# Performance work log

Measured on AMD Instinct MI355X. Metric: run time of the kernel, lower is better.

The kernel has to match this reference:

```python
import jax, jax.numpy as jnp
import numpy as np

SIZE = 128
WIN = SIZE // 4   # sliding-window size == region size (32)
HALF = WIN // 2   # 16


def _conv(x, w, pad, groups=1):
    return jax.lax.conv_general_dilated(x, w, (1, 1), [(pad, pad), (pad, pad)],
        dimension_numbers=('NCHW', 'OIHW', 'NCHW'), feature_group_count=groups)


def _resize(x, h, w):
    # F.interpolate(..., mode='bilinear', align_corners=False)
    return jax.image.resize(x, (x.shape[0], x.shape[1], h, w), 'bilinear', antialias=False)


def _gauss_kernels():
    ax = np.linspace(-2.0, 2.0, 5)
    xx, yy = np.meshgrid(ax, ax)
    g = np.exp(-(xx ** 2 + yy ** 2) / 2.0) / (2.0 * np.pi)  # sigma = 1
    gx = (-xx * g).astype(np.float32)
    gy = (-yy * g).astype(np.float32)
    return (jnp.asarray(np.tile(gx[None, None], (3, 3, 1, 1))),
            jnp.asarray(np.tile(gy[None, None], (3, 3, 1, 1))))


def _edge_extract(x):
    Gx, Gy = _gauss_kernels()
    h = _conv(x, Gx, 2)
    v = _conv(x, Gy, 2)
    return jnp.tanh(jnp.sqrt(h * h + v * v + 1e-8))


def _color_moments(x, win=5):
    # F.unfold-based local mean / unbiased var / skewness, via depthwise box sums
    C = x.shape[1]
    n = float(win * win)
    ones = jnp.ones((C, 1, win, win), x.dtype)
    box = lambda z: _conv(z, ones, win // 2, groups=C)
    s1 = box(x); s2 = box(x * x); s3 = box(x * x * x)
    mean = s1 / n
    var = (s2 - n * mean * mean) / (n - 1.0)               # unbiased, matches torch.var
    m3 = (s3 - 3.0 * mean * s2 + 2.0 * n * mean ** 3) / n  # E[(x-m)^3]
    skew = m3 / (jnp.sqrt(jnp.maximum(var, 0.0)) ** 3 + 1e-6)
    return jnp.concatenate([mean, var, skew], 1)


def _locate_region(c):
    # scipy: gradient magnitude < 0.2 -> 4-connected label at argmax -> bbox center
    H, W = c.shape
    flat = jnp.argmax(c)
    xm = (flat // W).astype(jnp.int32)
    ym = (flat % W).astype(jnp.int32)
    gm = jnp.hypot(jnp.gradient(c, axis=0), jnp.gradient(c, axis=1))
    mask = gm < 0.2
    seed = jnp.zeros((H, W), bool).at[xm, ym].set(True) & mask

    def dil(r):
        d = r
        d = d | jnp.pad(r[1:, :], ((0, 1), (0, 0)))
        d = d | jnp.pad(r[:-1, :], ((1, 0), (0, 0)))
        d = d | jnp.pad(r[:, 1:], ((0, 0), (0, 1)))
        d = d | jnp.pad(r[:, :-1], ((0, 0), (1, 0)))
        return d & mask

    def body(s):
        r, _ = s
        nr = dil(r)
        return (nr, jnp.any(nr != r))

    region, _ = jax.lax.while_loop(lambda s: s[1], body, (seed, jnp.any(seed)))
    rows = jnp.any(region, 1); cols = jnp.any(region, 0)
    rs = jnp.argmax(rows); re = H - jnp.argmax(rows[::-1])
    cs = jnp.argmax(cols); ce = W - jnp.argmax(cols[::-1])
    ok = mask[xm, ym]  # label_at_max != 0
    x1 = jnp.where(ok, ((rs + re) // 2).astype(jnp.int32), xm)
    y1 = jnp.where(ok, ((cs + ce) // 2).astype(jnp.int32), ym)
    return x1, y1


def _affine_grid(move, H, W):
    # theta = [[1,0,tx],[0,1,ty]] with (tx,ty)=move, align_corners=False
    bx = (2.0 * jnp.arange(W, dtype=jnp.float32) + 1.0) / W - 1.0
    by = (2.0 * jnp.arange(H, dtype=jnp.float32) + 1.0) / H - 1.0
    gx = bx[None, None, :] + move[:, 0, None, None]
    gy = by[None, :, None] + move[:, 1, None, None]
    return jnp.stack(jnp.broadcast_arrays(gx, gy), -1)  # [B,H,W,2]


def _grid_sample(x, grid):
    # bilinear, zeros padding, align_corners=False (torch defaults)
    B, C, H, W = x.shape
    ix = ((grid[..., 0] + 1.0) * W - 1.0) / 2.0
    iy = ((grid[..., 1] + 1.0) * H - 1.0) / 2.0
    ix0 = jnp.floor(ix).astype(jnp.int32)
    iy0 = jnp.floor(iy).astype(jnp.int32)
    wx1 = ix - ix0; wy1 = iy - iy0
    b = jnp.arange(B)[:, None, None]

    def g(yy, xx):
        valid = ((xx >= 0) & (xx < W) & (yy >= 0) & (yy < H)).astype(x.dtype)
        v = x[b, :, jnp.clip(yy, 0, H - 1), jnp.clip(xx, 0, W - 1)]  # [B,Hg,Wg,C]
        return v * valid[..., None]

    out = (g(iy0, ix0) * ((1 - wy1) * (1 - wx1))[..., None]
         + g(iy0, ix0 + 1) * ((1 - wy1) * wx1)[..., None]
         + g(iy0 + 1, ix0) * (wy1 * (1 - wx1))[..., None]
         + g(iy0 + 1, ix0 + 1) * (wy1 * wx1)[..., None])
    return jnp.transpose(out, (0, 3, 1, 2))


def _bn_relu6(x, w, b):
    # BatchNorm2d in training mode (batch stats, biased var, eps=1e-5) + ReLU6
    m = x.mean((0, 2, 3), keepdims=True)
    v = ((x - m) ** 2).mean((0, 2, 3), keepdims=True)
    y = (x - m) / jnp.sqrt(v + 1e-5) * w[None, :, None, None] + b[None, :, None, None]
    return jnp.clip(y, 0.0, 6.0)


def setup_inputs():
    key = jax.random.key(0)
    ks = jax.random.split(key, 8)
    B, C = 8, 64
    return dict(
        warm_flag=1,
        feat1=jax.random.normal(ks[0], (B, C, SIZE, SIZE), jnp.float32),
        feat2=jax.random.normal(ks[1], (B, C, SIZE, SIZE), jnp.float32),
        cam1=jax.random.uniform(ks[2], (B, 64, 64), jnp.float32),
        cam2=jax.random.uniform(ks[3], (B, 64, 64), jnp.float32),
        f_g=jax.random.uniform(ks[4], (B, 3, 512, 512), jnp.float32),
        f_e=jax.random.uniform(ks[5], (B, 3, 512, 512), jnp.float32),
        conv1_w=jax.random.normal(ks[6], (C, 3, 3, 3), jnp.float32) * 0.1,
        conv1_b=jnp.zeros((C,), jnp.float32),
        conv2_w=jax.random.normal(ks[7], (C, 9, 3, 3), jnp.float32) * 0.1,
        conv2_b=jnp.zeros((C,), jnp.float32),
        bn_w=jnp.ones((C,), jnp.float32),
        bn_b=jnp.zeros((C,), jnp.float32),
    )


def reference(warm_flag, feat1, feat2, cam1, cam2, f_g, f_e,
              conv1_w, conv1_b, conv2_w, conv2_b, bn_w, bn_b):
    B = cam1.shape[0]
    c1 = _resize(cam1[:, None], SIZE, SIZE)
    c2 = _resize(cam2[:, None], SIZE, SIZE)

    if warm_flag == 1:
        # numpy/scipy path in torch is detached from autograd
        c1s = jax.lax.stop_gradient(c1)
        c2s = jax.lax.stop_gradient(c2)
        x1, y1 = jax.vmap(_locate_region)(c1s[:, 0])
        # valid-mode box convolution of cam2 with ones((H//4, W//4)), argmax
        box = jax.lax.conv_general_dilated(c2s, jnp.ones((1, 1, WIN, WIN), c2.dtype), (1, 1),
            'VALID', dimension_numbers=('NCHW', 'OIHW', 'NCHW'))[:, 0]
        Wv = box.shape[-1]
        flat = jnp.argmax(box.reshape(B, -1), -1)
        x2 = (flat // Wv + HALF).astype(jnp.int32)
        y2 = (flat % Wv + HALF).astype(jnp.int32)

        idx = jnp.arange(SIZE)
        def rect(xc, yc):
            r = (idx[None, :] >= jnp.maximum(xc - HALF, 0)[:, None]) & \
                (idx[None, :] < jnp.minimum(xc + HALF, SIZE)[:, None])
            cc = (idx[None, :] >= jnp.maximum(yc - HALF, 0)[:, None]) & \
                 (idx[None, :] < jnp.minimum(yc + HALF, SIZE)[:, None])
            return r[:, None, :, None] & cc[:, None, None, :]
        mask1 = rect(x1, y1).astype(feat1.dtype)
        mask2 = rect(x2, y2).astype(feat2.dtype)
        mi1 = jnp.stack([x1, y1], -1).astype(jnp.float32)
        mi2 = jnp.stack([x2, y2], -1).astype(jnp.float32)
    else:
        mask1 = jnp.zeros_like(feat1)
        mask2 = jnp.zeros_like(feat2)
        mi1 = jnp.zeros((B, 2), jnp.float32)
        mi2 = jnp.zeros((B, 2), jnp.float32)

    cam2_move = (mi2 - mi1) / (SIZE // 2)
    cam1_move = (mi1 - mi2) / (SIZE // 2)
    grid1 = _affine_grid(cam1_move, SIZE, SIZE)
    grid2 = _affine_grid(cam2_move, SIZE, SIZE)

    moments = _resize(_color_moments(f_e), SIZE, SIZE)   # [B,9,128,128]
    edge = _resize(_edge_extract(f_g), SIZE, SIZE)       # [B,3,128,128]
    feat1_edge = jnp.clip(_conv(edge, conv1_w, 1) + conv1_b[None, :, None, None], 0.0, 6.0)
    feat2_color = _conv(moments, conv2_w, 1) + conv2_b[None, :, None, None]

    feat2_move = _grid_sample(feat2_color * mask2, grid2)
    feat1_edge_move = _grid_sample(feat1_edge * mask1, grid1)

    Bc, C, H, W = feat1.shape
    f1 = feat1.reshape(Bc, C, -1)
    f2 = feat2.reshape(Bc, C, -1)
    f2m = feat2_move.reshape(Bc, C, -1)
    f1m = feat1_edge_move.reshape(Bc, C, -1)

    f2_attn = jax.nn.softmax(jnp.einsum('bcn,bdn->bcd', f2m, f1), -1)  # [B,C,C]
    feat1_apply = jnp.einsum('bcd,bdn->bcn', f2_attn, f1).reshape(Bc, C, H, W)
    f1_attn = jax.nn.softmax(jnp.einsum('bcn,bdn->bcd', f1m, f2), -1)
    feat2_apply = jnp.einsum('bcd,bdn->bcn', f1_attn, f2).reshape(Bc, C, H, W)

    feat1_apply = _bn_relu6(feat1_apply, bn_w, bn_b)
    feat2_apply = _bn_relu6(feat2_apply, bn_w, bn_b)

    if warm_flag == 0:
        return (feat1, feat2, grid1, grid2, feat1_edge, feat2_color, f1_attn, f2_attn, feat1, feat2)
    return (feat1_apply, feat2_apply, grid1, grid2, feat1_edge, feat2_color, f1_attn, f2_attn, feat1, feat2)
```

## Files before the change

### kernel.cpp

```cpp
#include <hip/hip_runtime.h>
#include <math.h>

#define SIZE 128
#define WIN 32
#define HALF 16
#define B 8
#define C 64
#define N (SIZE*SIZE)
#define BCN 8388608
#define BV 97

#define O_APPLY1   0
#define O_APPLY2   8388608
#define O_GRID1    16777216
#define O_GRID2    17039360
#define O_EDGEF    17301504
#define O_COLORF   25690112
#define O_ATTN1    34078720
#define O_ATTN2    34111488
#define O_FEAT1    34144256
#define O_FEAT2    42532864

#define WS_BNP     0
#define WS_XY      361472
#define WS_MOM     361600
#define WS_EDGE    1541248
#define WS_BN      1737856

#define NEGINF (-3.402823466e+38f)

typedef unsigned __int128 u128;

__device__ __forceinline__ u128 hfill(u128 g, u128 m) {
  u128 p = m;
  g |= p & (g << 1);  p &= p << 1;
  g |= p & (g << 2);  p &= p << 2;
  g |= p & (g << 4);  p &= p << 4;
  g |= p & (g << 8);  p &= p << 8;
  g |= p & (g << 16); p &= p << 16;
  g |= p & (g << 32); p &= p << 32;
  g |= p & (g << 64);
  p = m;
  g |= p & (g >> 1);  p &= p >> 1;
  g |= p & (g >> 2);  p &= p >> 2;
  g |= p & (g >> 4);  p &= p >> 4;
  g |= p & (g >> 8);  p &= p >> 8;
  g |= p & (g >> 16); p &= p >> 16;
  g |= p & (g >> 32); p &= p >> 32;
  g |= p & (g >> 64);
  return g;
}

#define PREP_BASE 8
#define COPY_BASE 2056
#define COPY_HALF 8192
#define STAGE1_GRID (COPY_BASE + 2 * COPY_HALF)

__global__ __launch_bounds__(256) void k_stage1(
    const float* __restrict__ cam1, const float* __restrict__ cam2,
    int* __restrict__ xy, float* __restrict__ g1, float* __restrict__ g2,
    const float* __restrict__ fe, const float* __restrict__ fg,
    float* __restrict__ mom, float* __restrict__ edge,
    const float4* __restrict__ f1, float4* __restrict__ o8,
    const float4* __restrict__ f2, float4* __restrict__ o9) {
  __shared__ __align__(16) float smem[33824];
  int blk = blockIdx.x;
  int tid = threadIdx.x;

  if (blk >= COPY_BASE) {
    int c = blk - COPY_BASE;
    if (c < COPY_HALF) o8[c * 256 + tid] = f1[c * 256 + tid];
    else { int i = (c - COPY_HALF) * 256 + tid; o9[i] = f2[i]; }
    return;
  }

  if (blk >= PREP_BASE) {
    float* sx = smem;
    int pblk = blk - PREP_BASE;
    if (pblk < 1536) {
      int tile = pblk & 63, ch = (pblk >> 6) % 3, b = pblk / 192;
      int ti0 = (tile >> 3) * 16, tj0 = (tile & 7) * 16;
      const float* src = fe + (size_t)(b * 3 + ch) * 262144;
      int oy0 = 4 * ti0 - 1, ox0 = 4 * tj0 - 1;
      for (int l = tid; l < 66 * 66; l += 256) {
        int r = l / 66, cc = l % 66;
        int gy = oy0 + r, gx = ox0 + cc;
        sx[l] = (gy >= 0 && gy < 512 && gx >= 0 && gx < 512) ? src[gy * 512 + gx] : 0.f;
      }
      __syncthreads();
      int ii = tid >> 4, jj = tid & 15;
      int i = ti0 + ii, j = tj0 + jj;
      float s1a[6], s2a[6], s3a[6], s1b[6], s2b[6], s3b[6];
      #pragma unroll
      for (int t = 0; t < 6; ++t) {
        float a1 = 0, a2 = 0, a3 = 0, b1 = 0, b2 = 0, b3 = 0;
        int lx = 4 * jj + t;
        #pragma unroll
        for (int r = 0; r < 6; ++r) {
          float v = sx[(4 * ii + r) * 66 + lx];
          float v2 = v * v, v3 = v2 * v;
          if (r < 5) { a1 += v; a2 += v2; a3 += v3; }
          if (r > 0) { b1 += v; b2 += v2; b3 += v3; }
        }
        s1a[t] = a1; s2a[t] = a2; s3a[t] = a3;
        s1b[t] = b1; s2b[t] = b2; s3b[t] = b3;
      }
      float am = 0, av = 0, as = 0;
      #pragma unroll
      for (int py = 0; py < 2; ++py) {
        #pragma unroll
        for (int px = 0; px < 2; ++px) {
          float s1 = 0, s2 = 0, s3 = 0;
          #pragma unroll
          for (int t = 0; t < 5; ++t) {
            s1 += py ? s1b[px + t] : s1a[px + t];
            s2 += py ? s2b[px + t] : s2a[px + t];
            s3 += py ? s3b[px + t] : s3a[px + t];
          }
          float mean = s1 / 25.f;
          float var  = (s2 - 25.f * mean * mean) / 24.f;
          float m3   = (s3 - 3.f * mean * s2 + 50.f * mean * mean * mean) / 25.f;
          float sq   = sqrtf(fmaxf(var, 0.f));
          float skew = m3 / (sq * sq * sq + 1e-6f);
          am += mean; av += var; as += skew;
        }
      }
      int base = (b * 9 + ch) * N + i * 128 + j;
      mom[base]         = 0.25f * am;
      mom[base + 3 * N] = 0.25f * av;
      mom[base + 6 * N] = 0.25f * as;
    } else {
      int eblk = pblk - 1536;
      int tile = eblk & 63, b = eblk >> 6;
      int ti0 = (tile >> 3) * 16, tj0 = (tile & 7) * 16;
      const float* s0 = fg + (size_t)b * 3 * 262144;
      int oy0 = 4 * ti0 - 1, ox0 = 4 * tj0 - 1;
      for (int l = tid; l < 66 * 66; l += 256) {
        int r = l / 66, cc = l % 66;
        int gy = oy0 + r, gx = ox0 + cc;
        float v = 0.f;
        if (gy >= 0 && gy < 512 && gx >= 0 && gx < 512) {
          int o = gy * 512 + gx;
          v = s0[o] + s0[262144 + o] + s0[524288 + o];
        }
        sx[l] = v;
      }
      __syncthreads();
      int ii = tid >> 4, jj = tid & 15;
      int i = ti0 + ii, j = tj0 + jj;
      const float INV2PI = 0.15915494309189535f;
      float wg[5], ug[5];
      #pragma unroll
      for (int t = 0; t < 5; ++t) {
        float a = (float)t - 2.f;
        float e = expf(-0.5f * a * a);
        wg[t] = e; ug[t] = -a * e;
      }
      float rAa[6], rAb[6], rBa[6], rBb[6];
      #pragma unroll
      for (int t = 0; t < 6; ++t) {
        float aa = 0, ab = 0, ba = 0, bb = 0;
        int lx = 4 * jj + t;
        #pragma unroll
        for (int r = 0; r < 6; ++r) {
          float v = sx[(4 * ii + r) * 66 + lx];
          if (r < 5) { aa += v * wg[r]; ba += v * ug[r]; }
          if (r > 0) { ab += v * wg[r - 1]; bb += v * ug[r - 1]; }
        }
        rAa[t] = aa; rAb[t] = ab; rBa[t] = ba; rBb[t] = bb;
      }
      float acc = 0.f;
      #pragma unroll
      for (int py = 0; py < 2; ++py) {
        #pragma unroll
        for (int px = 0; px < 2; ++px) {
          float h = 0, v = 0;
          #pragma unroll
          for (int t = 0; t < 5; ++t) {
            float A  = py ? rAb[px + t] : rAa[px + t];
            float Bw = py ? rBb[px + t] : rBa[px + t];
            h += A * ug[t];
            v += Bw * wg[t];
          }
          h *= INV2PI; v *= INV2PI;
          acc += tanhf(sqrtf(h * h + v * v + 1e-8f));
        }
      }
      edge[b * N + i * 128 + j] = 0.25f * acc;
    }
    return;
  }

  float* sc  = smem;
  float* sc2 = smem + 16384;
  float* sv  = smem + 32768;
  int*   si  = (int*)(smem + 33024);
  unsigned long long* mask64 = (unsigned long long*)(smem + 33280);
  int* sint = (int*)(smem + 33792);
  int b = blk;
  const float* src1 = cam1 + b * 4096;
  const float* src2 = cam2 + b * 4096;

  float bv = NEGINF; int bi = 0;
  for (int k = 0; k < 64; ++k) {
    int pix = k * 256 + tid;
    int i = pix >> 7, j = pix & 127;
    float fy = fminf(fmaxf(0.5f * (float)i - 0.25f, 0.f), 63.f);
    float fx = fminf(fmaxf(0.5f * (float)j - 0.25f, 0.f), 63.f);
    int y0 = (int)fy; float ty = fy - (float)y0; int y1i = min(y0 + 1, 63);
    int x0 = (int)fx; float tx = fx - (float)x0; int x1i = min(x0 + 1, 63);
    float a00 = src1[y0 * 64 + x0],  a01 = src1[y0 * 64 + x1i];
    float a10 = src1[y1i * 64 + x0], a11 = src1[y1i * 64 + x1i];
    float v1 = (1.f - ty) * ((1.f - tx) * a00 + tx * a01)
             + ty * ((1.f - tx) * a10 + tx * a11);
    float c00 = src2[y0 * 64 + x0],  c01 = src2[y0 * 64 + x1i];
    float c10 = src2[y1i * 64 + x0], c11 = src2[y1i * 64 + x1i];
    float v2 = (1.f - ty) * ((1.f - tx) * c00 + tx * c01)
             + ty * ((1.f - tx) * c10 + tx * c11);
    sc[pix] = v1; sc2[pix] = v2;
    if (v1 > bv) { bv = v1; bi = pix; }
  }
  sv[tid] = bv; si[tid] = bi;
  __syncthreads();
  for (int s = 128; s; s >>= 1) {
    if (tid < s) {
      float ov = sv[tid + s]; int oi = si[tid + s];
      if (ov > sv[tid] || (ov == sv[tid] && oi < si[tid])) { sv[tid] = ov; si[tid] = oi; }
    }
    __syncthreads();
  }
  if (tid == 0) { sint[0] = si[0] >> 7; sint[1] = si[0] & 127; }
  __syncthreads();
  int s_xm = sint[0], s_ym = sint[1];

  for (int k = 0; k < 64; ++k) {
    int pix = k * 256 + tid;
    int i = pix >> 7, j = pix & 127;
    float gx_, gy_;
    if (i == 0)        gx_ = sc[128 + j] - sc[j];
    else if (i == 127) gx_ = sc[127 * 128 + j] - sc[126 * 128 + j];
    else               gx_ = 0.5f * (sc[(i + 1) * 128 + j] - sc[(i - 1) * 128 + j]);
    if (j == 0)        gy_ = sc[i * 128 + 1] - sc[i * 128];
    else if (j == 127) gy_ = sc[i * 128 + 127] - sc[i * 128 + 126];
    else               gy_ = 0.5f * (sc[i * 128 + j + 1] - sc[i * 128 + j - 1]);
    bool pred = hypotf(gx_, gy_) < 0.2f;
    unsigned long long bal = __ballot(pred);
    if ((tid & 63) == 0) mask64[(i << 1) + (j >> 6)] = bal;
  }
  __syncthreads();
  if (tid == 0) {
    unsigned long long wdd = mask64[(s_xm << 1) + (s_ym >> 6)];
    sint[2] = (int)((wdd >> (s_ym & 63)) & 1ull);
  }
  __syncthreads();
  int s_ok = sint[2];

  if (tid < 64) {
    int l = tid;
    u128 m0 = ((u128)mask64[4 * l])     | ((u128)mask64[4 * l + 1] << 64);
    u128 m1 = ((u128)mask64[4 * l + 2]) | ((u128)mask64[4 * l + 3] << 64);
    u128 g0 = 0, g1v = 0;
    if (s_ok && (s_xm >> 1) == l) {
      if ((s_xm & 1) == 0) g0  = ((u128)1) << s_ym;
      else                 g1v = ((u128)1) << s_ym;
    }
    g0  = hfill(g0 & m0, m0);
    g1v = hfill(g1v & m1, m1);
    for (;;) {
      unsigned long long ulo = __shfl_up((unsigned long long)g1v, 1);
      unsigned long long uhi = __shfl_up((unsigned long long)(g1v >> 64), 1);
      u128 up = (l > 0) ? (((u128)ulo) | ((u128)uhi << 64)) : (u128)0;
      unsigned long long dlo = __shfl_down((unsigned long long)g0, 1);
      unsigned long long dhi = __shfl_down((unsigned long long)(g0 >> 64), 1);
      u128 dn = (l < 63) ? (((u128)dlo) | ((u128)dhi << 64)) : (u128)0;
      u128 n0 = hfill((g0 | up | g1v) & m0, m0);
      u128 n1 = hfill((g1v | n0 | dn) & m1, m1);
      bool chg = (n0 != g0) || (n1 != g1v);
      g0 = n0; g1v = n1;
      if (!__any(chg)) break;
    }
    unsigned long long be = __ballot(g0 != 0);
    unsigned long long bo = __ballot(g1v != 0);
    unsigned long long cl = (unsigned long long)(g0 | g1v);
    unsigned long long chh = (unsigned long long)((g0 | g1v) >> 64);
    for (int off = 32; off; off >>= 1) {
      cl  |= __shfl_xor(cl, off);
      chh |= __shfl_xor(chh, off);
    }
    if (l == 0) {
      int rs = 0, re = 0, cs = 0, ce = 0;
      if (be | bo) {
        int af = be ? (__ffsll(be) - 1) : 1000;
        int bf = bo ? (__ffsll(bo) - 1) : 1000;
        rs = min(af * 2, bf * 2 + 1);
        int al = be ? (63 - __clzll(be)) : -1000;
        int bl = bo ? (63 - __clzll(bo)) : -1000;
        re = max(al * 2, bl * 2 + 1) + 1;
        cs = cl ? (__ffsll(cl) - 1) : 64 + (__ffsll(chh) - 1);
        ce = chh ? 128 - __clzll(chh) : 64 - __clzll(cl);
      }
      int x1, y1;
      if (s_ok) { x1 = (rs + re) >> 1; y1 = (cs + ce) >> 1; }
      else      { x1 = s_xm;           y1 = s_ym; }
      xy[b] = x1; xy[8 + b] = y1; sint[3] = x1; sint[4] = y1;
    }
  }
  __syncthreads();

  for (int idx = tid; idx < BV * 128; idx += 256) {
    int rr = idx >> 7, cc = idx & 127;
    float acc = 0.f;
    #pragma unroll
    for (int dy = 0; dy < WIN; ++dy) acc += sc2[(rr + dy) * 128 + cc];
    sc[idx] = acc;
  }
  __syncthreads();

  bv = NEGINF; bi = 0;
  for (int p = tid; p < BV * BV; p += 256) {
    int rr = p / BV, cc = p % BV;
    float s = 0.f;
    #pragma unroll
    for (int dx = 0; dx < WIN; ++dx) s += sc[rr * 128 + cc + dx];
    if (s > bv) { bv = s; bi = p; }
  }
  sv[tid] = bv; si[tid] = bi;
  __syncthreads();
  for (int s = 128; s; s >>= 1) {
    if (tid < s) {
      float ov = sv[tid + s]; int oi = si[tid + s];
      if (ov > sv[tid] || (ov == sv[tid] && oi < si[tid])) { sv[tid] = ov; si[tid] = oi; }
    }
    __syncthreads();
  }
  if (tid == 0) {
    int x2 = si[0] / BV + HALF, y2 = si[0] % BV + HALF;
    xy[16 + b] = x2; xy[24 + b] = y2; sint[5] = x2; sint[6] = y2;
  }
  __syncthreads();

  float x1f = (float)sint[3], y1f = (float)sint[4];
  float x2f = (float)sint[5], y2f = (float)sint[6];
  float m1x = (x1f - x2f) / 64.f, m1y = (y1f - y2f) / 64.f;
  float* g1b = g1 + (size_t)b * N * 2;
  float* g2b = g2 + (size_t)b * N * 2;
  for (int k = 0; k < 64; ++k) {
    int pix = k * 256 + tid;
    int h = pix >> 7, w = pix & 127;
    float bx = (2.f * (float)w + 1.f) / 128.f - 1.f;
    float by = (2.f * (float)h + 1.f) / 128.f - 1.f;
    g1b[pix * 2]     = bx + m1x; g1b[pix * 2 + 1] = by + m1y;
    g2b[pix * 2]     = bx - m1x; g2b[pix * 2 + 1] = by - m1y;
  }
}

__global__ __launch_bounds__(256) void k_conv12(
    const float* __restrict__ edge, const float* __restrict__ w1,
    const float* __restrict__ b1, float* __restrict__ o4,
    const float* __restrict__ mom, const float* __restrict__ w2,
    const float* __restrict__ b2, float* __restrict__ o5) {
  __shared__ float tin[9 * 324];
  __shared__ float wsm[64 * 84];
  int b = blockIdx.x >> 6, tile = blockIdx.x & 63;
  int ti0 = (tile >> 3) * 16, tj0 = (tile & 7) * 16;
  int tid = threadIdx.x;
  int i = tid >> 4, j = tid & 15;
  if (blockIdx.y == 0) {
    for (int l = tid; l < 324; l += 256) {
      int r = l / 18, cc = l % 18;
      int gi = ti0 + r - 1, gj = tj0 + cc - 1;
      tin[l] = (gi >= 0 && gi < 128 && gj >= 0 && gj < 128) ? edge[b * N + gi * 128 + gj] : 0.f;
    }
    for (int l = tid; l < 64 * 12; l += 256) {
      int o = l / 12, t = l % 12;
      wsm[l] = (t < 9) ? (w1[o * 27 + t] + w1[o * 27 + 9 + t] + w1[o * 27 + 18 + t]) : 0.f;
    }
    __syncthreads();
    float win[12];
    #pragma unroll
    for (int dy = 0; dy < 3; ++dy)
      #pragma unroll
      for (int dx = 0; dx < 3; ++dx)
        win[dy * 3 + dx] = tin[(i + dy) * 18 + (j + dx)];
    win[9] = 0.f; win[10] = 0.f; win[11] = 0.f;
    float* o = o4 + (size_t)b * C * N + (ti0 + i) * 128 + tj0 + j;
    for (int oc = 0; oc < C; ++oc) {
      const float4* wr = (const float4*)(wsm + oc * 12);
      float acc = b1[oc];
      #pragma unroll
      for (int q = 0; q < 3; ++q) {
        float4 w4 = wr[q];
        acc += w4.x * win[4 * q] + w4.y * win[4 * q + 1]
             + w4.z * win[4 * q + 2] + w4.w * win[4 * q + 3];
      }
      o[oc * N] = fminf(fmaxf(acc, 0.f), 6.f);
    }
  } else {
    for (int l = tid; l < 9 * 324; l += 256) {
      int ic = l / 324, rem = l % 324, r = rem / 18, cc = rem % 18;
      int gi = ti0 + r - 1, gj = tj0 + cc - 1;
      tin[l] = (gi >= 0 && gi < 128 && gj >= 0 && gj < 128) ? mom[(b * 9 + ic) * N + gi * 128 + gj] : 0.f;
    }
    for (int l = tid; l < 64 * 84; l += 256) {
      int o = l / 84, t = l % 84;
      wsm[l] = (t < 81) ? w2[o * 81 + t] : 0.f;
    }
    __syncthreads();
    float win[84];
    #pragma unroll
    for (int ic = 0; ic < 9; ++ic)
      #pragma unroll
      for (int dy = 0; dy < 3; ++dy)
        #pragma unroll
        for (int dx = 0; dx < 3; ++dx)
          win[ic * 9 + dy * 3 + dx] = tin[ic * 324 + (i + dy) * 18 + (j + dx)];
    win[81] = 0.f; win[82] = 0.f; win[83] = 0.f;
    float* o = o5 + (size_t)b * C * N + (ti0 + i) * 128 + tj0 + j;
    for (int oc = 0; oc < C; ++oc) {
      const float4* wr = (const float4*)(wsm + oc * 84);
      float acc = b2[oc];
      #pragma unroll
      for (int q = 0; q < 21; ++q) {
        float4 w4 = wr[q];
        acc += w4.x * win[4 * q] + w4.y * win[4 * q + 1]
             + w4.z * win[4 * q + 2] + w4.w * win[4 * q + 3];
      }
      o[oc * N] = acc;
    }
  }
}

__global__ __launch_bounds__(256) void k_logits(const float* __restrict__ aB1,
                                                const float* __restrict__ bB1,
                                                const float* __restrict__ aB2,
                                                const float* __restrict__ bB2,
                                                float* __restrict__ lg,
                                                const int* __restrict__ xy) {
  int mode = blockIdx.y;
  const float* aBase = mode ? aB2 : aB1;
  const float* bBase = mode ? bB2 : bB1;
  int b = blockIdx.x >> 4, sl = blockIdx.x & 15;
  int tid = threadIdx.x;
  int ci = (tid >> 4) << 2, di = (tid & 15) << 2;
  float* o = lg + (size_t)(((mode * 8 + b) * 16 + sl)) * 4096;

  int x1 = xy[b], y1 = xy[8 + b], x2 = xy[16 + b], y2 = xy[24 + b];
  int dyh, dxw, rlo, rhi, clo, chi;
  if (mode == 0) {
    dyh = y1 - y2; dxw = x1 - x2;
    rlo = max(x1 - HALF, 0); rhi = min(x1 + HALF, SIZE);
    clo = max(y1 - HALF, 0); chi = min(y1 + HALF, SIZE);
  } else {
    dyh = y2 - y1; dxw = x2 - x1;
    rlo = max(x2 - HALF, 0); rhi = min(x2 + HALF, SIZE);
    clo = max(y2 - HALF, 0); chi = min(y2 + HALF, SIZE);
  }
  int hlo = max(0, rlo - dyh), hhi = min(SIZE, rhi - dyh);
  int wlo = max(0, clo - dxw), whi = min(SIZE, chi - dxw);
  int wn = whi - wlo, hn = hhi - hlo;
  int npos = (wn > 0 && hn > 0) ? wn * hn : 0;
  if (sl * 64 >= npos) {
    #pragma unroll
    for (int u = 0; u < 4; ++u)
      #pragma unroll
      for (int v = 0; v < 4; ++v)
        o[(ci + u) * 64 + (di + v)] = 0.f;
    return;
  }

  __shared__ float aS[64][65];
  __shared__ float bS[64][65];
  const float* aB = aBase + (size_t)b * C * N;
  const float* bB = bBase + (size_t)b * C * N;
  for (int l = tid; l < 4096; l += 256) {
    int ch = l >> 6, k = l & 63;
    int p = sl * 64 + k;
    float av = 0.f, bv = 0.f;
    if (p < npos) {
      int h = hlo + p / wn, w = wlo + p % wn;
      av = aB[ch * N + (h + dyh) * 128 + (w + dxw)];
      bv = bB[ch * N + h * 128 + w];
    }
    aS[ch][k] = av; bS[ch][k] = bv;
  }
  __syncthreads();
  float acc[4][4] = {};
  #pragma unroll 4
  for (int k = 0; k < 64; ++k) {
    float a0 = aS[ci][k], a1 = aS[ci + 1][k], a2 = aS[ci + 2][k], a3 = aS[ci + 3][k];
    float b0 = bS[di][k], b1v = bS[di + 1][k], b2v = bS[di + 2][k], b3 = bS[di + 3][k];
    acc[0][0] += a0 * b0; acc[0][1] += a0 * b1v; acc[0][2] += a0 * b2v; acc[0][3] += a0 * b3;
    acc[1][0] += a1 * b0; acc[1][1] += a1 * b1v; acc[1][2] += a1 * b2v; acc[1][3] += a1 * b3;
    acc[2][0] += a2 * b0; acc[2][1] += a2 * b1v; acc[2][2] += a2 * b2v; acc[2][3] += a2 * b3;
    acc[3][0] += a3 * b0; acc[3][1] += a3 * b1v; acc[3][2] += a3 * b2v; acc[3][3] += a3 * b3;
  }
  #pragma unroll
  for (int u = 0; u < 4; ++u)
    #pragma unroll
    for (int v = 0; v < 4; ++v)
      o[(ci + u) * 64 + (di + v)] = acc[u][v];
}

__global__ void k_softmax(const float* __restrict__ lg,
                          float* __restrict__ o6, float* __restrict__ o7) {
  int row = blockIdx.x;
  int mode = blockIdx.y;
  float* dst = mode ? o7 : o6;
  int b = row >> 6, c = row & 63;
  int lane = threadIdx.x;
  const float* base = lg + (size_t)((mode * 8 + b) * 16) * 4096 + c * 64 + lane;
  float v = 0.f;
  #pragma unroll
  for (int sl = 0; sl < 16; ++sl) v += base[sl * 4096];
  float mx = v;
  for (int off = 32; off; off >>= 1) mx = fmaxf(mx, __shfl_xor(mx, off));
  float e = expf(v - mx);
  float s = e;
  for (int off = 32; off; off >>= 1) s += __shfl_xor(s, off);
  dst[row * 64 + lane] = e / s;
}

__global__ __launch_bounds__(256) void k_applyst(const float* __restrict__ a1,
                                                 const float* __restrict__ s1_,
                                                 float* __restrict__ d1,
                                                 const float* __restrict__ a2,
                                                 const float* __restrict__ s2_,
                                                 float* __restrict__ d2,
                                                 float* __restrict__ bnp) {
  const float* attn; const float* src; float* dst;
  int t = blockIdx.y;
  if (t == 0) { attn = a1; src = s1_; dst = d1; }
  else        { attn = a2; src = s2_; dst = d2; }
  int b = blockIdx.x >> 6, chunk = blockIdx.x & 63;
  int n0 = chunk * 256 + threadIdx.x;
  const float* s = src + (size_t)b * C * N + n0;
  float v[64];
  #pragma unroll
  for (int d = 0; d < 64; ++d) v[d] = s[d * N];
  const float4* at4 = (const float4*)(attn + b * 4096);
  float* o = dst + (size_t)b * C * N + n0;
  __shared__ float red[64][4], red2[64][4];
  int lane = threadIdx.x & 63, wave = threadIdx.x >> 6;
  for (int c = 0; c < 64; ++c) {
    float acc = 0.f;
    #pragma unroll
    for (int q = 0; q < 16; ++q) {
      float4 w4 = at4[c * 16 + q];
      acc += w4.x * v[4 * q] + w4.y * v[4 * q + 1] + w4.z * v[4 * q + 2] + w4.w * v[4 * q + 3];
    }
    o[c * N] = acc;
    float sr = acc, ssr = acc * acc;
    for (int off = 32; off; off >>= 1) {
      sr  += __shfl_xor(sr, off);
      ssr += __shfl_xor(ssr, off);
    }
    if (lane == 0) { red[c][wave] = sr; red2[c][wave] = ssr; }
  }
  __syncthreads();
  if (threadIdx.x < 64) {
    int c = threadIdx.x;
    float sr  = red[c][0] + red[c][1] + red[c][2] + red[c][3];
    float ssr = red2[c][0] + red2[c][1] + red2[c][2] + red2[c][3];
    int idx = (t * 64 + c) * 512 + blockIdx.x;
    bnp[idx]         = sr;
    bnp[65536 + idx] = ssr;
  }
}

__global__ void k_bnstats2(const float* __restrict__ bnp, float* __restrict__ stats) {
  __shared__ float sr[128][4], ssr[128][4];
  int tid = threadIdx.x;
  int combo = tid >> 2, q = tid & 3;
  float s = 0.f, ss = 0.f;
  for (int k = 0; k < 128; ++k) {
    int idx = combo * 512 + q * 128 + k;
    s  += bnp[idx];
    ss += bnp[65536 + idx];
  }
  sr[combo][q] = s; ssr[combo][q] = ss;
  __syncthreads();
  if (q == 0) {
    float S  = sr[combo][0] + sr[combo][1] + sr[combo][2] + sr[combo][3];
    float SS = ssr[combo][0] + ssr[combo][1] + ssr[combo][2] + ssr[combo][3];
    int t = combo >> 6, c = combo & 63;
    float mean = S / 131072.f;
    float var  = SS / 131072.f - mean * mean;
    stats[t * 128 + c]      = mean;
    stats[t * 128 + 64 + c] = 1.f / sqrtf(var + 1e-5f);
  }
}

__global__ __launch_bounds__(256) void k_bnapply(
    float4* __restrict__ o0, float4* __restrict__ o1,
    const float* __restrict__ stats,
    const float* __restrict__ bw, const float* __restrict__ bb) {
  int i = blockIdx.x * 256 + threadIdx.x;
  int t = blockIdx.y;
  float4* p = t ? o1 : o0;
  int c = (i >> 12) & 63;
  float m = stats[t * 128 + c], r = stats[t * 128 + 64 + c];
  float w_ = bw[c], b_ = bb[c];
  float4 v = p[i];
  v.x = fminf(fmaxf((v.x - m) * r * w_ + b_, 0.f), 6.f);
  v.y = fminf(fmaxf((v.y - m) * r * w_ + b_, 0.f), 6.f);
  v.z = fminf(fmaxf((v.z - m) * r * w_ + b_, 0.f), 6.f);
  v.w = fminf(fmaxf((v.w - m) * r * w_ + b_, 0.f), 6.f);
  p[i] = v;
}

extern "C" void kernel_launch(void* const* d_in, const int* in_sizes, int n_in,
                              void* d_out, int out_size, void* d_ws, size_t ws_size,
                              hipStream_t stream) {
  const float* feat1   = (const float*)d_in[1];
  const float* feat2   = (const float*)d_in[2];
  const float* cam1    = (const float*)d_in[3];
  const float* cam2    = (const float*)d_in[4];
  const float* f_g     = (const float*)d_in[5];
  const float* f_e     = (const float*)d_in[6];
  const float* conv1_w = (const float*)d_in[7];
  const float* conv1_b = (const float*)d_in[8];
  const float* conv2_w = (const float*)d_in[9];
  const float* conv2_b = (const float*)d_in[10];
  const float* bn_w    = (const float*)d_in[11];
  const float* bn_b    = (const float*)d_in[12];

  float* out = (float*)d_out;
  float* w = (float*)d_ws;
  int* xy = (int*)(w + WS_XY);

  float* o0 = out + O_APPLY1;
  float* o1 = out + O_APPLY2;
  float* o2 = out + O_GRID1;
  float* o3 = out + O_GRID2;
  float* o4 = out + O_EDGEF;
  float* o5 = out + O_COLORF;
  float* o6 = out + O_ATTN1;
  float* o7 = out + O_ATTN2;
  float* o8 = out + O_FEAT1;
  float* o9 = out + O_FEAT2;

  k_stage1<<<STAGE1_GRID, 256, 0, stream>>>(
      cam1, cam2, xy, o2, o3,
      f_e, f_g, w + WS_MOM, w + WS_EDGE,
      (const float4*)feat1, (float4*)o8, (const float4*)feat2, (float4*)o9);

  k_conv12<<<dim3(B * 64, 2), 256, 0, stream>>>(w + WS_EDGE, conv1_w, conv1_b, o4,
                                                w + WS_MOM, conv2_w, conv2_b, o5);

  k_logits<<<dim3(B * 16, 2), 256, 0, stream>>>(o4, feat2, o5, feat1,
                                                w + WS_MOM, xy);

  k_softmax<<<dim3(B * C, 2), 64, 0, stream>>>(w + WS_MOM, o6, o7);

  k_applyst<<<dim3(B * 64, 2), 256, 0, stream>>>(o7, feat1, o0, o6, feat2, o1,
                                                 w + WS_BNP);

  k_bnstats2<<<1, 512, 0, stream>>>(w + WS_BNP, w + WS_BN);

  k_bnapply<<<dim3(BCN / 4 / 256, 2), 256, 0, stream>>>(
      (float4*)o0, (float4*)o1, w + WS_BN, bn_w, bn_b);
}
```

Measured before the change: 590.7 us.

## Split per-batch region search across two block sets and move grid writes

The per-batch front-end block used to do both the cam1 connected-region search and the cam2 sliding-window argmax in sequence. These now run in separate blocks (8 extra), so the serial critical path of the slowest block in stage 1 gets shorter. Each block stages the 64x64 CAM into shared memory before bilinear upsampling, instead of doing four global gathers per pixel. The grid output writes move into extra blocks of the conv kernel, which reads xy from global memory. This adds a small amount of work to that kernel's launch.

```diff
diff --git a/kernel.cpp b/kernel.cpp
--- a/kernel.cpp
+++ b/kernel.cpp
@@ -51,14 +51,26 @@
   return g;
 }
 
-#define PREP_BASE 8
-#define COPY_BASE 2056
+__device__ __forceinline__ float resamp(const float* raw, int i, int j) {
+  float fy = fminf(fmaxf(0.5f * (float)i - 0.25f, 0.f), 63.f);
+  float fx = fminf(fmaxf(0.5f * (float)j - 0.25f, 0.f), 63.f);
+  int y0 = (int)fy; float ty = fy - (float)y0; int y1i = min(y0 + 1, 63);
+  int x0 = (int)fx; float tx = fx - (float)x0; int x1i = min(x0 + 1, 63);
+  float a00 = raw[y0 * 64 + x0],  a01 = raw[y0 * 64 + x1i];
+  float a10 = raw[y1i * 64 + x0], a11 = raw[y1i * 64 + x1i];
+  return (1.f - ty) * ((1.f - tx) * a00 + tx * a01)
+       + ty * ((1.f - tx) * a10 + tx * a11);
+}
+
+#define FRONT_B   8
+#define PREP_BASE 16
+#define COPY_BASE 2064
 #define COPY_HALF 8192
 #define STAGE1_GRID (COPY_BASE + 2 * COPY_HALF)
 
 __global__ __launch_bounds__(256) void k_stage1(
     const float* __restrict__ cam1, const float* __restrict__ cam2,
-    int* __restrict__ xy, float* __restrict__ g1, float* __restrict__ g2,
+    int* __restrict__ xy,
     const float* __restrict__ fe, const float* __restrict__ fg,
     float* __restrict__ mom, float* __restrict__ edge,
     const float4* __restrict__ f1, float4* __restrict__ o8,
@@ -191,166 +203,165 @@
     return;
   }
 
-  float* sc  = smem;
-  float* sc2 = smem + 16384;
-  float* sv  = smem + 32768;
-  int*   si  = (int*)(smem + 33024);
-  unsigned long long* mask64 = (unsigned long long*)(smem + 33280);
-  int* sint = (int*)(smem + 33792);
-  int b = blk;
-  const float* src1 = cam1 + b * 4096;
-  const float* src2 = cam2 + b * 4096;
-
-  float bv = NEGINF; int bi = 0;
-  for (int k = 0; k < 64; ++k) {
-    int pix = k * 256 + tid;
-    int i = pix >> 7, j = pix & 127;
-    float fy = fminf(fmaxf(0.5f * (float)i - 0.25f, 0.f), 63.f);
-    float fx = fminf(fmaxf(0.5f * (float)j - 0.25f, 0.f), 63.f);
-    int y0 = (int)fy; float ty = fy - (float)y0; int y1i = min(y0 + 1, 63);
-    int x0 = (int)fx; float tx = fx - (float)x0; int x1i = min(x0 + 1, 63);
-    float a00 = src1[y0 * 64 + x0],  a01 = src1[y0 * 64 + x1i];
-    float a10 = src1[y1i * 64 + x0], a11 = src1[y1i * 64 + x1i];
-    float v1 = (1.f - ty) * ((1.f - tx) * a00 + tx * a01)
-             + ty * ((1.f - tx) * a10 + tx * a11);
-    float c00 = src2[y0 * 64 + x0],  c01 = src2[y0 * 64 + x1i];
-    float c10 = src2[y1i * 64 + x0], c11 = src2[y1i * 64 + x1i];
-    float v2 = (1.f - ty) * ((1.f - tx) * c00 + tx * c01)
-             + ty * ((1.f - tx) * c10 + tx * c11);
-    sc[pix] = v1; sc2[pix] = v2;
-    if (v1 > bv) { bv = v1; bi = pix; }
-  }
-  sv[tid] = bv; si[tid] = bi;
-  __syncthreads();
-  for (int s = 128; s; s >>= 1) {
-    if (tid < s) {
-      float ov = sv[tid + s]; int oi = si[tid + s];
-      if (ov > sv[tid] || (ov == sv[tid] && oi < si[tid])) { sv[tid] = ov; si[tid] = oi; }
-    }
-    __syncthreads();
-  }
-  if (tid == 0) { sint[0] = si[0] >> 7; sint[1] = si[0] & 127; }
-  __syncthreads();
-  int s_xm = sint[0], s_ym = sint[1];
-
-  for (int k = 0; k < 64; ++k) {
-    int pix = k * 256 + tid;
-    int i = pix >> 7, j = pix & 127;
-    float gx_, gy_;
-    if (i == 0)        gx_ = sc[128 + j] - sc[j];
-    else if (i == 127) gx_ = sc[127 * 128 + j] - sc[126 * 128 + j];
-    else               gx_ = 0.5f * (sc[(i + 1) * 128 + j] - sc[(i - 1) * 128 + j]);
-    if (j == 0)        gy_ = sc[i * 128 + 1] - sc[i * 128];
-    else if (j == 127) gy_ = sc[i * 128 + 127] - sc[i * 128 + 126];
-    else               gy_ = 0.5f * (sc[i * 128 + j + 1] - sc[i * 128 + j - 1]);
-    bool pred = hypotf(gx_, gy_) < 0.2f;
-    unsigned long long bal = __ballot(pred);
-    if ((tid & 63) == 0) mask64[(i << 1) + (j >> 6)] = bal;
-  }
-  __syncthreads();
-  if (tid == 0) {
-    unsigned long long wdd = mask64[(s_xm << 1) + (s_ym >> 6)];
-    sint[2] = (int)((wdd >> (s_ym & 63)) & 1ull);
-  }
-  __syncthreads();
-  int s_ok = sint[2];
-
-  if (tid < 64) {
-    int l = tid;
-    u128 m0 = ((u128)mask64[4 * l])     | ((u128)mask64[4 * l + 1] << 64);
-    u128 m1 = ((u128)mask64[4 * l + 2]) | ((u128)mask64[4 * l + 3] << 64);
-    u128 g0 = 0, g1v = 0;
-    if (s_ok && (s_xm >> 1) == l) {
-      if ((s_xm & 1) == 0) g0  = ((u128)1) << s_ym;
-      else                 g1v = ((u128)1) << s_ym;
-    }
-    g0  = hfill(g0 & m0, m0);
-    g1v = hfill(g1v & m1, m1);
-    for (;;) {
-      unsigned long long ulo = __shfl_up((unsigned long long)g1v, 1);
-      unsigned long long uhi = __shfl_up((unsigned long long)(g1v >> 64), 1);
-      u128 up = (l > 0) ? (((u128)ulo) | ((u128)uhi << 64)) : (u128)0;
-      unsigned long long dlo = __shfl_down((unsigned long long)g0, 1);
-      unsigned long long dhi = __shfl_down((unsigned long long)(g0 >> 64), 1);
-      u128 dn = (l < 63) ? (((u128)dlo) | ((u128)dhi << 64)) : (u128)0;
-      u128 n0 = hfill((g0 | up | g1v) & m0, m0);
-      u128 n1 = hfill((g1v | n0 | dn) & m1, m1);
-      bool chg = (n0 != g0) || (n1 != g1v);
-      g0 = n0; g1v = n1;
-      if (!__any(chg)) break;
-    }
-    unsigned long long be = __ballot(g0 != 0);
-    unsigned long long bo = __ballot(g1v != 0);
-    unsigned long long cl = (unsigned long long)(g0 | g1v);
-    unsigned long long chh = (unsigned long long)((g0 | g1v) >> 64);
-    for (int off = 32; off; off >>= 1) {
-      cl  |= __shfl_xor(cl, off);
-      chh |= __shfl_xor(chh, off);
-    }
-    if (l == 0) {
-      int rs = 0, re = 0, cs = 0, ce = 0;
-      if (be | bo) {
-        int af = be ? (__ffsll(be) - 1) : 1000;
-        int bf = bo ? (__ffsll(bo) - 1) : 1000;
-        rs = min(af * 2, bf * 2 + 1);
-        int al = be ? (63 - __clzll(be)) : -1000;
-        int bl = bo ? (63 - __clzll(bo)) : -1000;
-        re = max(al * 2, bl * 2 + 1) + 1;
-        cs = cl ? (__ffsll(cl) - 1) : 64 + (__ffsll(chh) - 1);
-        ce = chh ? 128 - __clzll(chh) : 64 - __clzll(cl);
-      }
-      int x1, y1;
-      if (s_ok) { x1 = (rs + re) >> 1; y1 = (cs + ce) >> 1; }
-      else      { x1 = s_xm;           y1 = s_ym; }
-      xy[b] = x1; xy[8 + b] = y1; sint[3] = x1; sint[4] = y1;
-    }
-  }
-  __syncthreads();
-
-  for (int idx = tid; idx < BV * 128; idx += 256) {
-    int rr = idx >> 7, cc = idx & 127;
-    float acc = 0.f;
+  if (blk >= FRONT_B) {
+    int b = blk - FRONT_B;
+    float* raw = smem;
+    float* sc2 = smem + 4096;
+    float* cs  = smem + 20480;
+    float* sv  = smem + 32896;
+    int*   si  = (int*)(smem + 33152);
+
+    const float4* c4 = (const float4*)(cam2 + b * 4096);
+    float4* r4 = (float4*)raw;
     #pragma unroll
-    for (int dy = 0; dy < WIN; ++dy) acc += sc2[(rr + dy) * 128 + cc];
-    sc[idx] = acc;
-  }
-  __syncthreads();
-
-  bv = NEGINF; bi = 0;
-  for (int p = tid; p < BV * BV; p += 256) {
-    int rr = p / BV, cc = p % BV;
-    float s = 0.f;
+    for (int k = 0; k < 4; ++k) r4[k * 256 + tid] = c4[k * 256 + tid];
+    __syncthreads();
+    for (int k = 0; k < 64; ++k) {
+      int pix = k * 256 + tid;
+      sc2[pix] = resamp(raw, pix >> 7, pix & 127);
+    }
+    __syncthreads();
+
+    for (int idx = tid; idx < BV * 128; idx += 256) {
+      int rr = idx >> 7, cc = idx & 127;
+      float acc = 0.f;
+      #pragma unroll
+      for (int dy = 0; dy < WIN; ++dy) acc += sc2[(rr + dy) * 128 + cc];
+      cs[idx] = acc;
+    }
+    __syncthreads();
+
+    float bv = NEGINF; int bi = 0;
+    for (int p = tid; p < BV * BV; p += 256) {
+      int rr = p / BV, cc = p % BV;
+      float s = 0.f;
+      #pragma unroll
+      for (int dx = 0; dx < WIN; ++dx) s += cs[rr * 128 + cc + dx];
+      if (s > bv) { bv = s; bi = p; }
+    }
+    sv[tid] = bv; si[tid] = bi;
+    __syncthreads();
+    for (int s = 128; s; s >>= 1) {
+      if (tid < s) {
+        float ov = sv[tid + s]; int oi = si[tid + s];
+        if (ov > sv[tid] || (ov == sv[tid] && oi < si[tid])) { sv[tid] = ov; si[tid] = oi; }
+      }
+      __syncthreads();
+    }
+    if (tid == 0) {
+      xy[16 + b] = si[0] / BV + HALF;
+      xy[24 + b] = si[0] % BV + HALF;
+    }
+    return;
+  }
+
+  {
+    int b = blk;
+    float* raw = smem;
+    float* sc  = smem + 4096;
+    float* sv  = smem + 20480;
+    int*   si  = (int*)(smem + 20736);
+    unsigned long long* mask64 = (unsigned long long*)(smem + 20992);
+    int* sint = (int*)(smem + 21504);
+
+    const float4* c4 = (const float4*)(cam1 + b * 4096);
+    float4* r4 = (float4*)raw;
     #pragma unroll
-    for (int dx = 0; dx < WIN; ++dx) s += sc[rr * 128 + cc + dx];
-    if (s > bv) { bv = s; bi = p; }
-  }
-  sv[tid] = bv; si[tid] = bi;
-  __syncthreads();
-  for (int s = 128; s; s >>= 1) {
-    if (tid < s) {
-      float ov = sv[tid + s]; int oi = si[tid + s];
-      if (ov > sv[tid] || (ov == sv[tid] && oi < si[tid])) { sv[tid] = ov; si[tid] = oi; }
-    }
-    __syncthreads();
-  }
-  if (tid == 0) {
-    int x2 = si[0] / BV + HALF, y2 = si[0] % BV + HALF;
-    xy[16 + b] = x2; xy[24 + b] = y2; sint[5] = x2; sint[6] = y2;
-  }
-  __syncthreads();
-
-  float x1f = (float)sint[3], y1f = (float)sint[4];
-  float x2f = (float)sint[5], y2f = (float)sint[6];
-  float m1x = (x1f - x2f) / 64.f, m1y = (y1f - y2f) / 64.f;
-  float* g1b = g1 + (size_t)b * N * 2;
-  float* g2b = g2 + (size_t)b * N * 2;
-  for (int k = 0; k < 64; ++k) {
-    int pix = k * 256 + tid;
-    int h = pix >> 7, w = pix & 127;
-    float bx = (2.f * (float)w + 1.f) / 128.f - 1.f;
-    float by = (2.f * (float)h + 1.f) / 128.f - 1.f;
-    g1b[pix * 2]     = bx + m1x; g1b[pix * 2 + 1] = by + m1y;
-    g2b[pix * 2]     = bx - m1x; g2b[pix * 2 + 1] = by - m1y;
+    for (int k = 0; k < 4; ++k) r4[k * 256 + tid] = c4[k * 256 + tid];
+    __syncthreads();
+
+    float bv = NEGINF; int bi = 0;
+    for (int k = 0; k < 64; ++k) {
+      int pix = k * 256 + tid;
+      float v1 = resamp(raw, pix >> 7, pix & 127);
+      sc[pix] = v1;
+      if (v1 > bv) { bv = v1; bi = pix; }
+    }
+    sv[tid] = bv; si[tid] = bi;
+    __syncthreads();
+    for (int s = 128; s; s >>= 1) {
+      if (tid < s) {
+        float ov = sv[tid + s]; int oi = si[tid + s];
+        if (ov > sv[tid] || (ov == sv[tid] && oi < si[tid])) { sv[tid] = ov; si[tid] = oi; }
+      }
+      __syncthreads();
+    }
+    if (tid == 0) { sint[0] = si[0] >> 7; sint[1] = si[0] & 127; }
+    __syncthreads();
+    int s_xm = sint[0], s_ym = sint[1];
+
+    for (int k = 0; k < 64; ++k) {
+      int pix = k * 256 + tid;
+      int i = pix >> 7, j = pix & 127;
+      float gx_, gy_;
+      if (i == 0)        gx_ = sc[128 + j] - sc[j];
+      else if (i == 127) gx_ = sc[127 * 128 + j] - sc[126 * 128 + j];
+      else               gx_ = 0.5f * (sc[(i + 1) * 128 + j] - sc[(i - 1) * 128 + j]);
+      if (j == 0)        gy_ = sc[i * 128 + 1] - sc[i * 128];
+      else if (j == 127) gy_ = sc[i * 128 + 127] - sc[i * 128 + 126];
+      else               gy_ = 0.5f * (sc[i * 128 + j + 1] - sc[i * 128 + j - 1]);
+      bool pred = hypotf(gx_, gy_) < 0.2f;
+      unsigned long long bal = __ballot(pred);
+      if ((tid & 63) == 0) mask64[(i << 1) + (j >> 6)] = bal;
+    }
+    __syncthreads();
+    if (tid == 0) {
+      unsigned long long wdd = mask64[(s_xm << 1) + (s_ym >> 6)];
+      sint[2] = (int)((wdd >> (s_ym & 63)) & 1ull);
+    }
+    __syncthreads();
+    int s_ok = sint[2];
+
+    if (tid < 64) {
+      int l = tid;
+      u128 m0 = ((u128)mask64[4 * l])     | ((u128)mask64[4 * l + 1] << 64);
+      u128 m1 = ((u128)mask64[4 * l + 2]) | ((u128)mask64[4 * l + 3] << 64);
+      u128 g0 = 0, g1v = 0;
+      if (s_ok && (s_xm >> 1) == l) {
+        if ((s_xm & 1) == 0) g0  = ((u128)1) << s_ym;
+        else                 g1v = ((u128)1) << s_ym;
+      }
+      g0  = hfill(g0 & m0, m0);
+      g1v = hfill(g1v & m1, m1);
+      for (;;) {
+        unsigned long long ulo = __shfl_up((unsigned long long)g1v, 1);
+        unsigned long long uhi = __shfl_up((unsigned long long)(g1v >> 64), 1);
+        u128 up = (l > 0) ? (((u128)ulo) | ((u128)uhi << 64)) : (u128)0;
+        unsigned long long dlo = __shfl_down((unsigned long long)g0, 1);
+        unsigned long long dhi = __shfl_down((unsigned long long)(g0 >> 64), 1);
+        u128 dn = (l < 63) ? (((u128)dlo) | ((u128)dhi << 64)) : (u128)0;
+        u128 n0 = hfill((g0 | up | g1v) & m0, m0);
+        u128 n1 = hfill((g1v | n0 | dn) & m1, m1);
+        bool chg = (n0 != g0) || (n1 != g1v);
+        g0 = n0; g1v = n1;
+        if (!__any(chg)) break;
+      }
+      unsigned long long be = __ballot(g0 != 0);
+      unsigned long long bo = __ballot(g1v != 0);
+      unsigned long long cl = (unsigned long long)(g0 | g1v);
+      unsigned long long chh = (unsigned long long)((g0 | g1v) >> 64);
+      for (int off = 32; off; off >>= 1) {
+        cl  |= __shfl_xor(cl, off);
+        chh |= __shfl_xor(chh, off);
+      }
+      if (l == 0) {
+        int rs = 0, re = 0, cs_ = 0, ce = 0;
+        if (be | bo) {
+          int af = be ? (__ffsll(be) - 1) : 1000;
+          int bf = bo ? (__ffsll(bo) - 1) : 1000;
+          rs = min(af * 2, bf * 2 + 1);
+          int al = be ? (63 - __clzll(be)) : -1000;
+          int bl = bo ? (63 - __clzll(bo)) : -1000;
+          re = max(al * 2, bl * 2 + 1) + 1;
+          cs_ = cl ? (__ffsll(cl) - 1) : 64 + (__ffsll(chh) - 1);
+          ce = chh ? 128 - __clzll(chh) : 64 - __clzll(cl);
+        }
+        int x1, y1;
+        if (s_ok) { x1 = (rs + re) >> 1; y1 = (cs_ + ce) >> 1; }
+        else      { x1 = s_xm;           y1 = s_ym; }
+        xy[b] = x1; xy[8 + b] = y1;
+      }
+    }
   }
 }
 
@@ -358,12 +369,33 @@
     const float* __restrict__ edge, const float* __restrict__ w1,
     const float* __restrict__ b1, float* __restrict__ o4,
     const float* __restrict__ mom, const float* __restrict__ w2,
-    const float* __restrict__ b2, float* __restrict__ o5) {
+    const float* __restrict__ b2, float* __restrict__ o5,
+    const int* __restrict__ xy, float* __restrict__ g1, float* __restrict__ g2) {
   __shared__ float tin[9 * 324];
   __shared__ float wsm[64 * 84];
+  int tid = threadIdx.x;
+
+  if (blockIdx.x >= 512) {
+    if (blockIdx.y != 0) return;
+    int b = blockIdx.x - 512;
+    float x1f = (float)xy[b], y1f = (float)xy[8 + b];
+    float x2f = (float)xy[16 + b], y2f = (float)xy[24 + b];
+    float m1x = (x1f - x2f) / 64.f, m1y = (y1f - y2f) / 64.f;
+    float* g1b = g1 + (size_t)b * N * 2;
+    float* g2b = g2 + (size_t)b * N * 2;
+    for (int k = 0; k < 64; ++k) {
+      int pix = k * 256 + tid;
+      int h = pix >> 7, w = pix & 127;
+      float bx = (2.f * (float)w + 1.f) / 128.f - 1.f;
+      float by = (2.f * (float)h + 1.f) / 128.f - 1.f;
+      g1b[pix * 2]     = bx + m1x; g1b[pix * 2 + 1] = by + m1y;
+      g2b[pix * 2]     = bx - m1x; g2b[pix * 2 + 1] = by - m1y;
+    }
+    return;
+  }
+
   int b = blockIdx.x >> 6, tile = blockIdx.x & 63;
   int ti0 = (tile >> 3) * 16, tj0 = (tile & 7) * 16;
-  int tid = threadIdx.x;
   int i = tid >> 4, j = tid & 15;
   if (blockIdx.y == 0) {
     for (int l = tid; l < 324; l += 256) {
@@ -640,12 +672,13 @@
   float* o9 = out + O_FEAT2;
 
   k_stage1<<<STAGE1_GRID, 256, 0, stream>>>(
-      cam1, cam2, xy, o2, o3,
+      cam1, cam2, xy,
       f_e, f_g, w + WS_MOM, w + WS_EDGE,
       (const float4*)feat1, (float4*)o8, (const float4*)feat2, (float4*)o9);
 
-  k_conv12<<<dim3(B * 64, 2), 256, 0, stream>>>(w + WS_EDGE, conv1_w, conv1_b, o4,
-                                                w + WS_MOM, conv2_w, conv2_b, o5);
+  k_conv12<<<dim3(520, 2), 256, 0, stream>>>(w + WS_EDGE, conv1_w, conv1_b, o4,
+                                             w + WS_MOM, conv2_w, conv2_b, o5,
+                                             xy, o2, o3);
 
   k_logits<<<dim3(B * 16, 2), 256, 0, stream>>>(o4, feat2, o5, feat1,
                                                 w + WS_MOM, xy);
```

New measurement: 587.7 us. About the same (-0.5%).
